# Performance work log

Hardware: AMD Instinct MI355X
Metric: run time of the kernel (lower is better)

## Reference

```python
import jax, jax.numpy as jnp
import numpy as np

N = 50000
E = 500000
H = 128


def setup_inputs() -> dict:
    key = jax.random.key(0)
    ks = jax.random.split(key, 7)
    x = jax.random.normal(ks[0], (N, 4, H), dtype=jnp.float32)
    edge_index = jax.random.randint(ks[1], (2, E), 0, N, dtype=jnp.int64)
    s = 1.0 / np.sqrt(H)
    W_s_rel = jax.random.normal(ks[2], (H, H), dtype=jnp.float32) * s
    W_s_root = jax.random.normal(ks[3], (H, H), dtype=jnp.float32) * s
    b_s_root = jax.random.normal(ks[4], (H,), dtype=jnp.float32) * s
    W_v_rel = jax.random.normal(ks[5], (H, H), dtype=jnp.float32) * s
    W_v_root = jax.random.normal(ks[6], (H, H), dtype=jnp.float32) * s
    return {"x": x, "edge_index": edge_index, "W_s_rel": W_s_rel,
            "W_s_root": W_s_root, "b_s_root": b_s_root,
            "W_v_rel": W_v_rel, "W_v_root": W_v_root}


def reference(x, edge_index, W_s_rel, W_s_root, b_s_root, W_v_rel, W_v_root):
    # x: (N, 4, H); channel 0 is scalar, channels 1:4 are a 3-vector per feature
    scalar = x[:, 0, :]          # (N, H)
    vector = x[:, 1:, :]         # (N, 3, H)
    row, col = edge_index[0], edge_index[1]
    n = scalar.shape[0]

    # Per-edge messages: gather source (col) features, project with rel weights
    scalar_msg = scalar[col] @ W_s_rel.T                     # (E, H)
    vector_msg = jnp.einsum('evh,oh->evo', vector[col], W_v_rel)  # (E, 3, H)

    # Scatter-add into destination (row) nodes
    scalar_agg = jax.ops.segment_sum(scalar_msg, row, num_segments=n)
    vector_agg = jax.ops.segment_sum(vector_msg, row, num_segments=n)

    scalar_out = scalar @ W_s_root.T + b_s_root + scalar_agg          # (N, H)
    vector_out = jnp.einsum('nvh,oh->nvo', vector, W_v_root) + vector_agg  # (N, 3, H)

    return jnp.concatenate([scalar_out[:, None, :], vector_out], axis=1)  # (N, 4, H)
```

## Files before the change

kernel.cpp:

```cpp
#include <hip/hip_runtime.h>


typedef short bfrag __attribute__((ext_vector_type(8)));
typedef float cfrag __attribute__((ext_vector_type(16)));
typedef float f4v  __attribute__((ext_vector_type(4)));

__device__ __forceinline__ short f2bf(float f) {
    unsigned u = __builtin_bit_cast(unsigned, f);
    u += 0x7fff + ((u >> 16) & 1);
    return (short)(u >> 16);
}
__device__ __forceinline__ float bf2f(short s) {
    unsigned u = ((unsigned)(unsigned short)s) << 16;
    return __builtin_bit_cast(float, u);
}
__device__ __forceinline__ bfrag pack8(float4 lo, float4 hi) {
    bfrag r;
    r[0] = f2bf(lo.x); r[1] = f2bf(lo.y); r[2] = f2bf(lo.z); r[3] = f2bf(lo.w);
    r[4] = f2bf(hi.x); r[5] = f2bf(hi.y); r[6] = f2bf(hi.z); r[7] = f2bf(hi.w);
    return r;
}
__device__ __forceinline__ bfrag pack8v(f4v lo, f4v hi) {
    bfrag r;
    r[0] = f2bf(lo[0]); r[1] = f2bf(lo[1]); r[2] = f2bf(lo[2]); r[3] = f2bf(lo[3]);
    r[4] = f2bf(hi[0]); r[5] = f2bf(hi[1]); r[6] = f2bf(hi[2]); r[7] = f2bf(hi[3]);
    return r;
}

__global__ __launch_bounds__(256) void hist_kernel(
    const int* __restrict__ ei, int* __restrict__ counts, int E)
{
    int e = blockIdx.x * 256 + threadIdx.x;
    if (e < E) atomicAdd(&counts[ei[e]], 1);
}

__global__ __launch_bounds__(1024) void scan_local_kernel(
    const int* __restrict__ counts, int* __restrict__ offsets,
    int* __restrict__ blocksums, int N)
{
    __shared__ int wsum[16];
    const int tid = threadIdx.x, lane = tid & 63, wid = tid >> 6;
    int i = blockIdx.x * 1024 + tid;
    int v = (i < N) ? counts[i] : 0;
    int incl = v;
    #pragma unroll
    for (int off = 1; off < 64; off <<= 1) {
        int t = __shfl_up(incl, off, 64);
        if (lane >= off) incl += t;
    }
    if (lane == 63) wsum[wid] = incl;
    __syncthreads();
    if (wid == 0) {
        int ws = (lane < 16) ? wsum[lane] : 0;
        int wincl = ws;
        #pragma unroll
        for (int off = 1; off < 16; off <<= 1) {
            int t = __shfl_up(wincl, off, 64);
            if (lane >= off) wincl += t;
        }
        if (lane < 16) wsum[lane] = wincl - ws;
    }
    __syncthreads();
    int excl = incl - v + wsum[wid];
    if (i < N) offsets[i] = excl;
    if (tid == 1023) blocksums[blockIdx.x] = excl + v;
}

__global__ __launch_bounds__(64) void scan_blocksums_kernel(
    int* __restrict__ bs, int nb)
{
    int lane = threadIdx.x;
    int v = (lane < nb) ? bs[lane] : 0;
    int incl = v;
    #pragma unroll
    for (int off = 1; off < 64; off <<= 1) {
        int t = __shfl_up(incl, off, 64);
        if (lane >= off) incl += t;
    }
    if (lane < nb) bs[lane] = incl - v;
}

__global__ __launch_bounds__(1024) void scan_add_kernel(
    int* __restrict__ offsets, int* __restrict__ cursor,
    const int* __restrict__ bs, int N, int E)
{
    int i = blockIdx.x * 1024 + threadIdx.x;
    if (i < N) {
        int v = offsets[i] + bs[blockIdx.x];
        offsets[i] = v;
        cursor[i] = v;
    }
    if (i == 0) offsets[N] = E;
}

__global__ __launch_bounds__(256) void bin_kernel(
    const int* __restrict__ ei, int* __restrict__ cursor,
    int* __restrict__ bins, int E)
{
    int e = blockIdx.x * 256 + threadIdx.x;
    if (e < E) {
        int row = ei[e], col = ei[E + e];
        int pos = atomicAdd(&cursor[row], 1);
        bins[pos] = col;
    }
}

__global__ __launch_bounds__(256) void conv_x_kernel(
    const float* __restrict__ x, short* __restrict__ xbf, long long total8)
{
    long long i = (long long)blockIdx.x * 256 + threadIdx.x;
    if (i >= total8) return;
    f4v lo = __builtin_nontemporal_load((const f4v*)(x + i * 8));
    f4v hi = __builtin_nontemporal_load((const f4v*)(x + i * 8 + 4));
    *(bfrag*)(xbf + i * 8) = pack8v(lo, hi);
}

__global__ __launch_bounds__(256) void conv_w_kernel(
    const float* __restrict__ w0, const float* __restrict__ w1,
    const float* __restrict__ w2, const float* __restrict__ w3,
    short* __restrict__ wbf)
{
    int i = blockIdx.x * 256 + threadIdx.x;
    int j = i * 8;
    int m = j >> 14, off = j & 16383;
    const float* src = (m == 0) ? w0 : (m == 1) ? w1 : (m == 2) ? w2 : w3;
    float4 lo = *(const float4*)(src + off);
    float4 hi = *(const float4*)(src + off + 4);
    *(bfrag*)(wbf + j) = pack8(lo, hi);
}

template<int XBF>
__global__ __launch_bounds__(256) void fused_agg_mfma(
    const float* __restrict__ x, const short* __restrict__ xbf,
    const int* __restrict__ offsets, const int* __restrict__ bins,
    float* __restrict__ out, const short* __restrict__ wbf,
    const float* __restrict__ b_s, int Nn)
{
    __shared__ short atile[32 * 512];
    const int tid  = threadIdx.x;
    const int wid  = tid >> 6;
    const int lane = tid & 63;
    const int n0   = blockIdx.x * 32;

    const int cl   = lane >> 4;
    const int slot = lane & 15;
    #pragma unroll 1
    for (int i = 0; i < 8; i++) {
        const int m = wid * 8 + i;
        const int n = n0 + m;
        float acc[8] = {0, 0, 0, 0, 0, 0, 0, 0};
        if (n < Nn) {
            const int beg = offsets[n], end = offsets[n + 1];
            int e = beg;
            if (XBF) {
                for (; e + 8 <= end; e += 8) {
                    int cc[8];
                    #pragma unroll
                    for (int q = 0; q < 8; q++) cc[q] = bins[e + q];
                    bfrag v[8];
                    #pragma unroll
                    for (int q = 0; q < 8; q++)
                        v[q] = *(const bfrag*)(xbf + (size_t)cc[q] * 512 + lane * 8);
                    #pragma unroll
                    for (int j = 0; j < 8; j++)
                        acc[j] += ((bf2f(v[0][j]) + bf2f(v[1][j])) +
                                   (bf2f(v[2][j]) + bf2f(v[3][j]))) +
                                  ((bf2f(v[4][j]) + bf2f(v[5][j])) +
                                   (bf2f(v[6][j]) + bf2f(v[7][j])));
                }
                for (; e + 4 <= end; e += 4) {
                    int cc[4];
                    #pragma unroll
                    for (int q = 0; q < 4; q++) cc[q] = bins[e + q];
                    bfrag v[4];
                    #pragma unroll
                    for (int q = 0; q < 4; q++)
                        v[q] = *(const bfrag*)(xbf + (size_t)cc[q] * 512 + lane * 8);
                    #pragma unroll
                    for (int j = 0; j < 8; j++)
                        acc[j] += (bf2f(v[0][j]) + bf2f(v[1][j])) +
                                  (bf2f(v[2][j]) + bf2f(v[3][j]));
                }
                for (; e < end; e++) {
                    int cc = bins[e];
                    bfrag v = *(const bfrag*)(xbf + (size_t)cc * 512 + lane * 8);
                    #pragma unroll
                    for (int j = 0; j < 8; j++) acc[j] += bf2f(v[j]);
                }
            } else {
                for (; e < end; e++) {
                    int cc = bins[e];
                    float4 l = *(const float4*)(x + (size_t)cc * 512 + lane * 8);
                    float4 h = *(const float4*)(x + (size_t)cc * 512 + lane * 8 + 4);
                    acc[0] += l.x; acc[1] += l.y; acc[2] += l.z; acc[3] += l.w;
                    acc[4] += h.x; acc[5] += h.y; acc[6] += h.z; acc[7] += h.w;
                }
            }
        }
        const int boff = m * 1024 + cl * 256 + ((slot * 16) ^ ((m & 15) << 4));
        *(bfrag*)((char*)atile + boff) =
            pack8(make_float4(acc[0], acc[1], acc[2], acc[3]),
                  make_float4(acc[4], acc[5], acc[6], acc[7]));
    }

    const int c   = wid;
    const int l31 = lane & 31;
    const int kg  = lane >> 5;
    int mA = n0 + l31; if (mA >= Nn) mA = Nn - 1;
    const size_t arow = ((size_t)mA * 4 + c) * 128;
    bfrag a0[8];
    #pragma unroll
    for (int ks = 0; ks < 8; ks++) {
        const int k0 = ks * 16 + kg * 8;
        if (XBF) {
            a0[ks] = *(const bfrag*)(xbf + arow + k0);
        } else {
            float4 lo = *(const float4*)(x + arow + k0);
            float4 hi = *(const float4*)(x + arow + k0 + 4);
            a0[ks] = pack8(lo, hi);
        }
    }

    __syncthreads();

    const short* wroot = wbf + ((c == 0) ? 0 : 2) * 16384;
    const short* wrel  = wbf + ((c == 0) ? 1 : 3) * 16384;

    cfrag acc4[4];
    #pragma unroll
    for (int t = 0; t < 4; t++)
        #pragma unroll
        for (int r = 0; r < 16; r++) acc4[t][r] = 0.f;

    #pragma unroll
    for (int ks = 0; ks < 8; ks++) {
        const int k0 = ks * 16 + kg * 8;
        const int rboff = l31 * 1024 + c * 256 + ((k0 * 2) ^ ((l31 & 15) << 4));
        bfrag a1 = *(const bfrag*)((const char*)atile + rboff);
        #pragma unroll
        for (int t = 0; t < 4; t++) {
            bfrag b0 = *(const bfrag*)(wroot + (size_t)(t * 32 + l31) * 128 + k0);
            acc4[t] = __builtin_amdgcn_mfma_f32_32x32x16_bf16(a0[ks], b0, acc4[t], 0, 0, 0);
            bfrag b1 = *(const bfrag*)(wrel + (size_t)(t * 32 + l31) * 128 + k0);
            acc4[t] = __builtin_amdgcn_mfma_f32_32x32x16_bf16(a1, b1, acc4[t], 0, 0, 0);
        }
    }

    float bv[4] = {0.f, 0.f, 0.f, 0.f};
    if (c == 0) {
        #pragma unroll
        for (int t = 0; t < 4; t++) bv[t] = b_s[t * 32 + l31];
    }

    #pragma unroll
    for (int t = 0; t < 4; t++) {
        #pragma unroll
        for (int r = 0; r < 16; r++) {
            int row = (r & 3) + 8 * (r >> 2) + 4 * kg;
            int node = n0 + row;
            if (node < Nn)
                __builtin_nontemporal_store(
                    acc4[t][r] + bv[t],
                    out + ((size_t)node * 4 + c) * 128 + t * 32 + l31);
        }
    }
}

extern "C" void kernel_launch(void* const* d_in, const int* in_sizes, int n_in,
                              void* d_out, int out_size, void* d_ws, size_t ws_size,
                              hipStream_t stream) {
    const float* x        = (const float*)d_in[0];
    const int*   ei       = (const int*)d_in[1];
    const float* W_s_rel  = (const float*)d_in[2];
    const float* W_s_root = (const float*)d_in[3];
    const float* b_s_root = (const float*)d_in[4];
    const float* W_v_rel  = (const float*)d_in[5];
    const float* W_v_root = (const float*)d_in[6];
    float* out = (float*)d_out;

    int N = in_sizes[0] / 512;
    int E = in_sizes[1] / 2;

    size_t ints_bytes = ((size_t)(3 * N + 1) + E + 64) * sizeof(int);
    size_t wbf_bytes  = 65536 * sizeof(short);
    size_t xbf_bytes  = (size_t)N * 512 * sizeof(short);
    bool use_bf = (ws_size >= wbf_bytes + xbf_bytes + ints_bytes);

    short* wbf = (short*)d_ws;
    short* xbf = wbf + 65536;
    int* counts = use_bf ? (int*)(xbf + (size_t)N * 512) : (int*)xbf;
    int* offsets   = counts + N;
    int* cursor    = offsets + N + 1;
    int* bins      = cursor + N;
    int* blocksums = bins + E;

    int nb = (N + 1023) / 1024;

    hipMemsetAsync(counts, 0, (size_t)N * sizeof(int), stream);
    hist_kernel<<<(E + 255) / 256, 256, 0, stream>>>(ei, counts, E);
    scan_local_kernel<<<nb, 1024, 0, stream>>>(counts, offsets, blocksums, N);
    scan_blocksums_kernel<<<1, 64, 0, stream>>>(blocksums, nb);
    scan_add_kernel<<<nb, 1024, 0, stream>>>(offsets, cursor, blocksums, N, E);
    bin_kernel<<<(E + 255) / 256, 256, 0, stream>>>(ei, cursor, bins, E);

    conv_w_kernel<<<32, 256, 0, stream>>>(W_s_root, W_s_rel, W_v_root, W_v_rel, wbf);

    if (use_bf) {
        long long total8 = (long long)N * 64;
        conv_x_kernel<<<(int)((total8 + 255) / 256), 256, 0, stream>>>(x, xbf, total8);
        fused_agg_mfma<1><<<(N + 31) / 32, 256, 0, stream>>>(
            x, xbf, offsets, bins, out, wbf, b_s_root, N);
    } else {
        fused_agg_mfma<0><<<(N + 31) / 32, 256, 0, stream>>>(
            x, nullptr, offsets, bins, out, wbf, b_s_root, N);
    }
}
```

Baseline: 384.8 us.

## Shrink node tile to 16 with 16x16x32 MFMA, fuse prep kernels, prefetch bins

The fused aggregation kernel now processes 16 nodes per block instead of 32. It switches from 32x32x16 to 16x16x32 bf16 MFMA and adds a launch-bounds occupancy hint, which halves LDS per block and allows more resident blocks. The x/weight bf16 conversion and the degree histogram are merged into a single prep kernel to cut launch overhead. The edge gather loop software-prefetches the next 8 bin indices, and MFMA sections raise wave priority. The trade-off is twice as many blocks, each re-reading the weights from global/L2, and more register pressure from the prefetch.

Measured after the change: 419.4 us. 9.0% more time.

```diff
diff --git a/kernel.cpp b/kernel.cpp
--- a/kernel.cpp
+++ b/kernel.cpp
@@ -2,7 +2,7 @@
 
 
 typedef short bfrag __attribute__((ext_vector_type(8)));
-typedef float cfrag __attribute__((ext_vector_type(16)));
+typedef float cfrag4 __attribute__((ext_vector_type(4)));
 typedef float f4v  __attribute__((ext_vector_type(4)));
 
 __device__ __forceinline__ short f2bf(float f) {
@@ -27,13 +27,6 @@
     return r;
 }
 
-__global__ __launch_bounds__(256) void hist_kernel(
-    const int* __restrict__ ei, int* __restrict__ counts, int E)
-{
-    int e = blockIdx.x * 256 + threadIdx.x;
-    if (e < E) atomicAdd(&counts[ei[e]], 1);
-}
-
 __global__ __launch_bounds__(1024) void scan_local_kernel(
     const int* __restrict__ counts, int* __restrict__ offsets,
     int* __restrict__ blocksums, int N)
@@ -105,58 +98,72 @@
     }
 }
 
-__global__ __launch_bounds__(256) void conv_x_kernel(
-    const float* __restrict__ x, short* __restrict__ xbf, long long total8)
-{
-    long long i = (long long)blockIdx.x * 256 + threadIdx.x;
-    if (i >= total8) return;
-    f4v lo = __builtin_nontemporal_load((const f4v*)(x + i * 8));
-    f4v hi = __builtin_nontemporal_load((const f4v*)(x + i * 8 + 4));
-    *(bfrag*)(xbf + i * 8) = pack8v(lo, hi);
-}
-
-__global__ __launch_bounds__(256) void conv_w_kernel(
+__global__ __launch_bounds__(256) void prep_kernel(
+    const float* __restrict__ x, short* __restrict__ xbf, long long total8,
     const float* __restrict__ w0, const float* __restrict__ w1,
     const float* __restrict__ w2, const float* __restrict__ w3,
-    short* __restrict__ wbf)
-{
-    int i = blockIdx.x * 256 + threadIdx.x;
-    int j = i * 8;
-    int m = j >> 14, off = j & 16383;
-    const float* src = (m == 0) ? w0 : (m == 1) ? w1 : (m == 2) ? w2 : w3;
-    float4 lo = *(const float4*)(src + off);
-    float4 hi = *(const float4*)(src + off + 4);
-    *(bfrag*)(wbf + j) = pack8(lo, hi);
+    short* __restrict__ wbf,
+    const int* __restrict__ ei, int* __restrict__ counts, int E,
+    int convB)
+{
+    int b = blockIdx.x;
+    if (b < convB) {
+        long long i = (long long)b * 256 + threadIdx.x;
+        if (i >= total8) return;
+        f4v lo = __builtin_nontemporal_load((const f4v*)(x + i * 8));
+        f4v hi = __builtin_nontemporal_load((const f4v*)(x + i * 8 + 4));
+        *(bfrag*)(xbf + i * 8) = pack8v(lo, hi);
+    } else if (b < convB + 32) {
+        int i = (b - convB) * 256 + threadIdx.x;
+        int j = i * 8;
+        int m = j >> 14, off = j & 16383;
+        const float* src = (m == 0) ? w0 : (m == 1) ? w1 : (m == 2) ? w2 : w3;
+        float4 lo = *(const float4*)(src + off);
+        float4 hi = *(const float4*)(src + off + 4);
+        *(bfrag*)(wbf + j) = pack8(lo, hi);
+    } else {
+        int e = (b - convB - 32) * 256 + threadIdx.x;
+        if (e < E) atomicAdd(&counts[ei[e]], 1);
+    }
 }
 
 template<int XBF>
-__global__ __launch_bounds__(256) void fused_agg_mfma(
+__global__ __launch_bounds__(256, 6) void fused_agg_mfma(
     const float* __restrict__ x, const short* __restrict__ xbf,
     const int* __restrict__ offsets, const int* __restrict__ bins,
     float* __restrict__ out, const short* __restrict__ wbf,
     const float* __restrict__ b_s, int Nn)
 {
-    __shared__ short atile[32 * 512];
+    __shared__ short atile[16 * 512];
     const int tid  = threadIdx.x;
     const int wid  = tid >> 6;
     const int lane = tid & 63;
-    const int n0   = blockIdx.x * 32;
+    const int n0   = blockIdx.x * 16;
 
     const int cl   = lane >> 4;
     const int slot = lane & 15;
     #pragma unroll 1
-    for (int i = 0; i < 8; i++) {
-        const int m = wid * 8 + i;
+    for (int i = 0; i < 4; i++) {
+        const int m = wid * 4 + i;
         const int n = n0 + m;
         float acc[8] = {0, 0, 0, 0, 0, 0, 0, 0};
         if (n < Nn) {
             const int beg = offsets[n], end = offsets[n + 1];
             int e = beg;
             if (XBF) {
-                for (; e + 8 <= end; e += 8) {
-                    int cc[8];
+                int cc[8];
+                bool have = (e + 8 <= end);
+                if (have) {
                     #pragma unroll
                     for (int q = 0; q < 8; q++) cc[q] = bins[e + q];
+                }
+                while (have) {
+                    int cn[8];
+                    const bool more = (e + 16 <= end);
+                    if (more) {
+                        #pragma unroll
+                        for (int q = 0; q < 8; q++) cn[q] = bins[e + 8 + q];
+                    }
                     bfrag v[8];
                     #pragma unroll
                     for (int q = 0; q < 8; q++)
@@ -167,31 +174,35 @@
                                    (bf2f(v[2][j]) + bf2f(v[3][j]))) +
                                   ((bf2f(v[4][j]) + bf2f(v[5][j])) +
                                    (bf2f(v[6][j]) + bf2f(v[7][j])));
+                    e += 8;
+                    #pragma unroll
+                    for (int q = 0; q < 8; q++) cc[q] = cn[q];
+                    have = more;
                 }
                 for (; e + 4 <= end; e += 4) {
-                    int cc[4];
-                    #pragma unroll
-                    for (int q = 0; q < 4; q++) cc[q] = bins[e + q];
+                    int c4[4];
+                    #pragma unroll
+                    for (int q = 0; q < 4; q++) c4[q] = bins[e + q];
                     bfrag v[4];
                     #pragma unroll
                     for (int q = 0; q < 4; q++)
-                        v[q] = *(const bfrag*)(xbf + (size_t)cc[q] * 512 + lane * 8);
+                        v[q] = *(const bfrag*)(xbf + (size_t)c4[q] * 512 + lane * 8);
                     #pragma unroll
                     for (int j = 0; j < 8; j++)
                         acc[j] += (bf2f(v[0][j]) + bf2f(v[1][j])) +
                                   (bf2f(v[2][j]) + bf2f(v[3][j]));
                 }
                 for (; e < end; e++) {
-                    int cc = bins[e];
-                    bfrag v = *(const bfrag*)(xbf + (size_t)cc * 512 + lane * 8);
+                    int cc1 = bins[e];
+                    bfrag v = *(const bfrag*)(xbf + (size_t)cc1 * 512 + lane * 8);
                     #pragma unroll
                     for (int j = 0; j < 8; j++) acc[j] += bf2f(v[j]);
                 }
             } else {
                 for (; e < end; e++) {
-                    int cc = bins[e];
-                    float4 l = *(const float4*)(x + (size_t)cc * 512 + lane * 8);
-                    float4 h = *(const float4*)(x + (size_t)cc * 512 + lane * 8 + 4);
+                    int cc1 = bins[e];
+                    float4 l = *(const float4*)(x + (size_t)cc1 * 512 + lane * 8);
+                    float4 h = *(const float4*)(x + (size_t)cc1 * 512 + lane * 8 + 4);
                     acc[0] += l.x; acc[1] += l.y; acc[2] += l.z; acc[3] += l.w;
                     acc[4] += h.x; acc[5] += h.y; acc[6] += h.z; acc[7] += h.w;
                 }
@@ -204,14 +215,14 @@
     }
 
     const int c   = wid;
-    const int l31 = lane & 31;
-    const int kg  = lane >> 5;
-    int mA = n0 + l31; if (mA >= Nn) mA = Nn - 1;
+    const int l15 = lane & 15;
+    const int kg  = lane >> 4;
+    int mA = n0 + l15; if (mA >= Nn) mA = Nn - 1;
     const size_t arow = ((size_t)mA * 4 + c) * 128;
-    bfrag a0[8];
-    #pragma unroll
-    for (int ks = 0; ks < 8; ks++) {
-        const int k0 = ks * 16 + kg * 8;
+    bfrag a0[4];
+    #pragma unroll
+    for (int ks = 0; ks < 4; ks++) {
+        const int k0 = ks * 32 + kg * 8;
         if (XBF) {
             a0[ks] = *(const bfrag*)(xbf + arow + k0);
         } else {
@@ -226,42 +237,46 @@
     const short* wroot = wbf + ((c == 0) ? 0 : 2) * 16384;
     const short* wrel  = wbf + ((c == 0) ? 1 : 3) * 16384;
 
-    cfrag acc4[4];
-    #pragma unroll
-    for (int t = 0; t < 4; t++)
-        #pragma unroll
-        for (int r = 0; r < 16; r++) acc4[t][r] = 0.f;
-
-    #pragma unroll
-    for (int ks = 0; ks < 8; ks++) {
-        const int k0 = ks * 16 + kg * 8;
-        const int rboff = l31 * 1024 + c * 256 + ((k0 * 2) ^ ((l31 & 15) << 4));
+    cfrag4 acc4[8];
+    #pragma unroll
+    for (int t = 0; t < 8; t++)
+        #pragma unroll
+        for (int r = 0; r < 4; r++) acc4[t][r] = 0.f;
+
+    __builtin_amdgcn_s_setprio(1);
+    #pragma unroll
+    for (int ks = 0; ks < 4; ks++) {
+        const int k0 = ks * 32 + kg * 8;
+        const int s = ks * 4 + kg;
+        const int rboff = l15 * 1024 + c * 256 + ((s * 16) ^ (l15 << 4));
         bfrag a1 = *(const bfrag*)((const char*)atile + rboff);
         #pragma unroll
-        for (int t = 0; t < 4; t++) {
-            bfrag b0 = *(const bfrag*)(wroot + (size_t)(t * 32 + l31) * 128 + k0);
-            acc4[t] = __builtin_amdgcn_mfma_f32_32x32x16_bf16(a0[ks], b0, acc4[t], 0, 0, 0);
-            bfrag b1 = *(const bfrag*)(wrel + (size_t)(t * 32 + l31) * 128 + k0);
-            acc4[t] = __builtin_amdgcn_mfma_f32_32x32x16_bf16(a1, b1, acc4[t], 0, 0, 0);
-        }
-    }
-
-    float bv[4] = {0.f, 0.f, 0.f, 0.f};
+        for (int t = 0; t < 8; t++) {
+            bfrag b0 = *(const bfrag*)(wroot + (size_t)(t * 16 + l15) * 128 + k0);
+            acc4[t] = __builtin_amdgcn_mfma_f32_16x16x32_bf16(a0[ks], b0, acc4[t], 0, 0, 0);
+            bfrag b1 = *(const bfrag*)(wrel + (size_t)(t * 16 + l15) * 128 + k0);
+            acc4[t] = __builtin_amdgcn_mfma_f32_16x16x32_bf16(a1, b1, acc4[t], 0, 0, 0);
+        }
+    }
+    __builtin_amdgcn_s_setprio(0);
+
+    float bv[8];
+    #pragma unroll
+    for (int t = 0; t < 8; t++) bv[t] = 0.f;
     if (c == 0) {
         #pragma unroll
-        for (int t = 0; t < 4; t++) bv[t] = b_s[t * 32 + l31];
-    }
-
-    #pragma unroll
-    for (int t = 0; t < 4; t++) {
-        #pragma unroll
-        for (int r = 0; r < 16; r++) {
-            int row = (r & 3) + 8 * (r >> 2) + 4 * kg;
-            int node = n0 + row;
+        for (int t = 0; t < 8; t++) bv[t] = b_s[t * 16 + l15];
+    }
+
+    #pragma unroll
+    for (int t = 0; t < 8; t++) {
+        #pragma unroll
+        for (int r = 0; r < 4; r++) {
+            int node = n0 + kg * 4 + r;
             if (node < Nn)
                 __builtin_nontemporal_store(
                     acc4[t][r] + bv[t],
-                    out + ((size_t)node * 4 + c) * 128 + t * 32 + l31);
+                    out + ((size_t)node * 4 + c) * 128 + t * 16 + l15);
         }
     }
 }
@@ -295,23 +310,24 @@
     int* blocksums = bins + E;
 
     int nb = (N + 1023) / 1024;
+    long long total8 = (long long)N * 64;
+    int convB = use_bf ? (int)((total8 + 255) / 256) : 0;
+    int nh = (E + 255) / 256;
 
     hipMemsetAsync(counts, 0, (size_t)N * sizeof(int), stream);
-    hist_kernel<<<(E + 255) / 256, 256, 0, stream>>>(ei, counts, E);
+    prep_kernel<<<convB + 32 + nh, 256, 0, stream>>>(
+        x, xbf, total8, W_s_root, W_s_rel, W_v_root, W_v_rel, wbf,
+        ei, counts, E, convB);
     scan_local_kernel<<<nb, 1024, 0, stream>>>(counts, offsets, blocksums, N);
     scan_blocksums_kernel<<<1, 64, 0, stream>>>(blocksums, nb);
     scan_add_kernel<<<nb, 1024, 0, stream>>>(offsets, cursor, blocksums, N, E);
     bin_kernel<<<(E + 255) / 256, 256, 0, stream>>>(ei, cursor, bins, E);
 
-    conv_w_kernel<<<32, 256, 0, stream>>>(W_s_root, W_s_rel, W_v_root, W_v_rel, wbf);
-
     if (use_bf) {
-        long long total8 = (long long)N * 64;
-        conv_x_kernel<<<(int)((total8 + 255) / 256), 256, 0, stream>>>(x, xbf, total8);
-        fused_agg_mfma<1><<<(N + 31) / 32, 256, 0, stream>>>(
+        fused_agg_mfma<1><<<(N + 15) / 16, 256, 0, stream>>>(
             x, xbf, offsets, bins, out, wbf, b_s_root, N);
     } else {
-        fused_agg_mfma<0><<<(N + 31) / 32, 256, 0, stream>>>(
+        fused_agg_mfma<0><<<(N + 15) / 16, 256, 0, stream>>>(
             x, nullptr, offsets, bins, out, wbf, b_s_root, N);
     }
 }
```

## Merge prep kernels, use single-block scan, raise MFMA wave priority

Applied to the files above, without the earlier changes.

The x conversion, weight conversion and histogram kernels are merged into one launch that dispatches by block-index range. The three-kernel scan is replaced by a single-block scan that loops over N with a carried prefix. Wave priority is raised around the MFMA loop. The aim is to cut launch count and inter-kernel gaps, at the cost of a serialized single-block scan over about 50 chunks.

Result: slower. 421.7 us (+9.6%).

```diff
diff --git a/kernel.cpp b/kernel.cpp
--- a/kernel.cpp
+++ b/kernel.cpp
@@ -27,70 +27,73 @@
     return r;
 }
 
-__global__ __launch_bounds__(256) void hist_kernel(
-    const int* __restrict__ ei, int* __restrict__ counts, int E)
-{
-    int e = blockIdx.x * 256 + threadIdx.x;
-    if (e < E) atomicAdd(&counts[ei[e]], 1);
-}
-
-__global__ __launch_bounds__(1024) void scan_local_kernel(
+__global__ __launch_bounds__(256) void prep_kernel(
+    const float* __restrict__ x, short* __restrict__ xbf, long long total8,
+    const float* __restrict__ w0, const float* __restrict__ w1,
+    const float* __restrict__ w2, const float* __restrict__ w3,
+    short* __restrict__ wbf,
+    const int* __restrict__ ei, int* __restrict__ counts, int E,
+    int convB)
+{
+    int b = blockIdx.x;
+    if (b < convB) {
+        long long i = (long long)b * 256 + threadIdx.x;
+        if (i >= total8) return;
+        f4v lo = __builtin_nontemporal_load((const f4v*)(x + i * 8));
+        f4v hi = __builtin_nontemporal_load((const f4v*)(x + i * 8 + 4));
+        *(bfrag*)(xbf + i * 8) = pack8v(lo, hi);
+    } else if (b < convB + 32) {
+        int i = (b - convB) * 256 + threadIdx.x;
+        int j = i * 8;
+        int m = j >> 14, off = j & 16383;
+        const float* src = (m == 0) ? w0 : (m == 1) ? w1 : (m == 2) ? w2 : w3;
+        float4 lo = *(const float4*)(src + off);
+        float4 hi = *(const float4*)(src + off + 4);
+        *(bfrag*)(wbf + j) = pack8(lo, hi);
+    } else {
+        int e = (b - convB - 32) * 256 + threadIdx.x;
+        if (e < E) atomicAdd(&counts[ei[e]], 1);
+    }
+}
+
+__global__ __launch_bounds__(1024) void scan_all_kernel(
     const int* __restrict__ counts, int* __restrict__ offsets,
-    int* __restrict__ blocksums, int N)
+    int* __restrict__ cursor, int N, int E)
 {
     __shared__ int wsum[16];
+    __shared__ int carry;
     const int tid = threadIdx.x, lane = tid & 63, wid = tid >> 6;
-    int i = blockIdx.x * 1024 + tid;
-    int v = (i < N) ? counts[i] : 0;
-    int incl = v;
-    #pragma unroll
-    for (int off = 1; off < 64; off <<= 1) {
-        int t = __shfl_up(incl, off, 64);
-        if (lane >= off) incl += t;
-    }
-    if (lane == 63) wsum[wid] = incl;
+    if (tid == 0) carry = 0;
     __syncthreads();
-    if (wid == 0) {
-        int ws = (lane < 16) ? wsum[lane] : 0;
-        int wincl = ws;
-        #pragma unroll
-        for (int off = 1; off < 16; off <<= 1) {
-            int t = __shfl_up(wincl, off, 64);
-            if (lane >= off) wincl += t;
-        }
-        if (lane < 16) wsum[lane] = wincl - ws;
-    }
-    __syncthreads();
-    int excl = incl - v + wsum[wid];
-    if (i < N) offsets[i] = excl;
-    if (tid == 1023) blocksums[blockIdx.x] = excl + v;
-}
-
-__global__ __launch_bounds__(64) void scan_blocksums_kernel(
-    int* __restrict__ bs, int nb)
-{
-    int lane = threadIdx.x;
-    int v = (lane < nb) ? bs[lane] : 0;
-    int incl = v;
-    #pragma unroll
-    for (int off = 1; off < 64; off <<= 1) {
-        int t = __shfl_up(incl, off, 64);
-        if (lane >= off) incl += t;
-    }
-    if (lane < nb) bs[lane] = incl - v;
-}
-
-__global__ __launch_bounds__(1024) void scan_add_kernel(
-    int* __restrict__ offsets, int* __restrict__ cursor,
-    const int* __restrict__ bs, int N, int E)
-{
-    int i = blockIdx.x * 1024 + threadIdx.x;
-    if (i < N) {
-        int v = offsets[i] + bs[blockIdx.x];
-        offsets[i] = v;
-        cursor[i] = v;
-    }
-    if (i == 0) offsets[N] = E;
+    for (int base = 0; base < N; base += 1024) {
+        int i = base + tid;
+        int v = (i < N) ? counts[i] : 0;
+        int incl = v;
+        #pragma unroll
+        for (int off = 1; off < 64; off <<= 1) {
+            int t = __shfl_up(incl, off, 64);
+            if (lane >= off) incl += t;
+        }
+        if (lane == 63) wsum[wid] = incl;
+        __syncthreads();
+        if (wid == 0) {
+            int ws = (lane < 16) ? wsum[lane] : 0;
+            int wincl = ws;
+            #pragma unroll
+            for (int off = 1; off < 16; off <<= 1) {
+                int t = __shfl_up(wincl, off, 64);
+                if (lane >= off) wincl += t;
+            }
+            if (lane < 16) wsum[lane] = wincl - ws;
+        }
+        __syncthreads();
+        int excl = incl - v + wsum[wid] + carry;
+        if (i < N) { offsets[i] = excl; cursor[i] = excl; }
+        __syncthreads();
+        if (tid == 1023) carry += incl + wsum[15];
+        __syncthreads();
+    }
+    if (tid == 0) offsets[N] = E;
 }
 
 __global__ __launch_bounds__(256) void bin_kernel(
@@ -103,30 +106,6 @@
         int pos = atomicAdd(&cursor[row], 1);
         bins[pos] = col;
     }
-}
-
-__global__ __launch_bounds__(256) void conv_x_kernel(
-    const float* __restrict__ x, short* __restrict__ xbf, long long total8)
-{
-    long long i = (long long)blockIdx.x * 256 + threadIdx.x;
-    if (i >= total8) return;
-    f4v lo = __builtin_nontemporal_load((const f4v*)(x + i * 8));
-    f4v hi = __builtin_nontemporal_load((const f4v*)(x + i * 8 + 4));
-    *(bfrag*)(xbf + i * 8) = pack8v(lo, hi);
-}
-
-__global__ __launch_bounds__(256) void conv_w_kernel(
-    const float* __restrict__ w0, const float* __restrict__ w1,
-    const float* __restrict__ w2, const float* __restrict__ w3,
-    short* __restrict__ wbf)
-{
-    int i = blockIdx.x * 256 + threadIdx.x;
-    int j = i * 8;
-    int m = j >> 14, off = j & 16383;
-    const float* src = (m == 0) ? w0 : (m == 1) ? w1 : (m == 2) ? w2 : w3;
-    float4 lo = *(const float4*)(src + off);
-    float4 hi = *(const float4*)(src + off + 4);
-    *(bfrag*)(wbf + j) = pack8(lo, hi);
 }
 
 template<int XBF>
@@ -169,29 +148,29 @@
                                    (bf2f(v[6][j]) + bf2f(v[7][j])));
                 }
                 for (; e + 4 <= end; e += 4) {
-                    int cc[4];
-                    #pragma unroll
-                    for (int q = 0; q < 4; q++) cc[q] = bins[e + q];
+                    int c4[4];
+                    #pragma unroll
+                    for (int q = 0; q < 4; q++) c4[q] = bins[e + q];
                     bfrag v[4];
                     #pragma unroll
                     for (int q = 0; q < 4; q++)
-                        v[q] = *(const bfrag*)(xbf + (size_t)cc[q] * 512 + lane * 8);
+                        v[q] = *(const bfrag*)(xbf + (size_t)c4[q] * 512 + lane * 8);
                     #pragma unroll
                     for (int j = 0; j < 8; j++)
                         acc[j] += (bf2f(v[0][j]) + bf2f(v[1][j])) +
                                   (bf2f(v[2][j]) + bf2f(v[3][j]));
                 }
                 for (; e < end; e++) {
-                    int cc = bins[e];
-                    bfrag v = *(const bfrag*)(xbf + (size_t)cc * 512 + lane * 8);
+                    int cc1 = bins[e];
+                    bfrag v = *(const bfrag*)(xbf + (size_t)cc1 * 512 + lane * 8);
                     #pragma unroll
                     for (int j = 0; j < 8; j++) acc[j] += bf2f(v[j]);
                 }
             } else {
                 for (; e < end; e++) {
-                    int cc = bins[e];
-                    float4 l = *(const float4*)(x + (size_t)cc * 512 + lane * 8);
-                    float4 h = *(const float4*)(x + (size_t)cc * 512 + lane * 8 + 4);
+                    int cc1 = bins[e];
+                    float4 l = *(const float4*)(x + (size_t)cc1 * 512 + lane * 8);
+                    float4 h = *(const float4*)(x + (size_t)cc1 * 512 + lane * 8 + 4);
                     acc[0] += l.x; acc[1] += l.y; acc[2] += l.z; acc[3] += l.w;
                     acc[4] += h.x; acc[5] += h.y; acc[6] += h.z; acc[7] += h.w;
                 }
@@ -232,6 +211,7 @@
         #pragma unroll
         for (int r = 0; r < 16; r++) acc4[t][r] = 0.f;
 
+    __builtin_amdgcn_s_setprio(1);
     #pragma unroll
     for (int ks = 0; ks < 8; ks++) {
         const int k0 = ks * 16 + kg * 8;
@@ -245,6 +225,7 @@
             acc4[t] = __builtin_amdgcn_mfma_f32_32x32x16_bf16(a1, b1, acc4[t], 0, 0, 0);
         }
     }
+    __builtin_amdgcn_s_setprio(0);
 
     float bv[4] = {0.f, 0.f, 0.f, 0.f};
     if (c == 0) {
@@ -292,22 +273,19 @@
     int* offsets   = counts + N;
     int* cursor    = offsets + N + 1;
     int* bins      = cursor + N;
-    int* blocksums = bins + E;
-
-    int nb = (N + 1023) / 1024;
+
+    long long total8 = (long long)N * 64;
+    int convB = use_bf ? (int)((total8 + 255) / 256) : 0;
+    int nh = (E + 255) / 256;
 
     hipMemsetAsync(counts, 0, (size_t)N * sizeof(int), stream);
-    hist_kernel<<<(E + 255) / 256, 256, 0, stream>>>(ei, counts, E);
-    scan_local_kernel<<<nb, 1024, 0, stream>>>(counts, offsets, blocksums, N);
-    scan_blocksums_kernel<<<1, 64, 0, stream>>>(blocksums, nb);
-    scan_add_kernel<<<nb, 1024, 0, stream>>>(offsets, cursor, blocksums, N, E);
+    prep_kernel<<<convB + 32 + nh, 256, 0, stream>>>(
+        x, xbf, total8, W_s_root, W_s_rel, W_v_root, W_v_rel, wbf,
+        ei, counts, E, convB);
+    scan_all_kernel<<<1, 1024, 0, stream>>>(counts, offsets, cursor, N, E);
     bin_kernel<<<(E + 255) / 256, 256, 0, stream>>>(ei, cursor, bins, E);
 
-    conv_w_kernel<<<32, 256, 0, stream>>>(W_s_root, W_s_rel, W_v_root, W_v_rel, wbf);
-
     if (use_bf) {
-        long long total8 = (long long)N * 64;
-        conv_x_kernel<<<(int)((total8 + 255) / 256), 256, 0, stream>>>(x, xbf, total8);
         fused_agg_mfma<1><<<(N + 31) / 32, 256, 0, stream>>>(
             x, xbf, offsets, bins, out, wbf, b_s_root, N);
     } else {
```
